# Kernel optimization log

Hardware: AMD Instinct MI355X
Metric: run time of the kernel (lower is better)

## Reference

```python
import jax, jax.numpy as jnp
import numpy as np
import math

# Module hyperparameters (match init_kwargs)
N_LEVELS = 16
LOG2_T = 19
T = 2 ** LOG2_T
BASE = (16, 16)
FINEST = (512, 512)
NUM_HASHGRID = 2
N_POINTS = 1_000_000
PRIME_Y = np.uint32(2654435761)  # standard NGP spatial-hash prime for the 2nd dim


def _resolutions():
    # replicate torch: int(base * b**i) per axis
    b_w = math.exp((math.log(FINEST[0]) - math.log(BASE[0])) / (N_LEVELS - 1))
    b_h = math.exp((math.log(FINEST[1]) - math.log(BASE[1])) / (N_LEVELS - 1))
    res_w = [int(BASE[0] * b_w ** i) for i in range(N_LEVELS)]
    res_h = [int(BASE[1] * b_h ** i) for i in range(N_LEVELS)]
    return jnp.array(np.stack([res_w, res_h], axis=-1), dtype=jnp.int32)  # [L,2]


def setup_inputs() -> dict:
    key = jax.random.key(0)
    k1, k2, k3 = jax.random.split(key, 3)
    x = jax.random.uniform(k1, (N_POINTS, 2), dtype=jnp.float32)
    hash_idxs = jax.random.randint(k2, (N_POINTS, 1), 0, NUM_HASHGRID, dtype=jnp.int32)
    # xavier-normal-like init of the hash tables [G, L, T, F]
    fan_in = N_LEVELS * T * 2
    fan_out = NUM_HASHGRID * T * 2
    std = math.sqrt(2.0 / (fan_in + fan_out))
    features = jax.random.normal(k3, (NUM_HASHGRID, N_LEVELS, T, 2), dtype=jnp.float32) * std
    return {"x": x, "features": features, "hash_idxs": hash_idxs}


def reference(x, features, hash_idxs):
    N = x.shape[0]
    res = _resolutions()                              # [L,2] int32
    scale = (res - 1).astype(jnp.float32)             # [L,2]
    pos = x[:, None, :] * scale[None]                 # [N,L,2]
    i0f = jnp.floor(pos)
    w = pos - i0f                                     # bilinear fractions [N,L,2]
    i0 = i0f.astype(jnp.int32).astype(jnp.uint32)     # [N,L,2]

    # 4 corner offsets: (0,0),(1,0),(0,1),(1,1)
    offs = jnp.array([[0, 0], [1, 0], [0, 1], [1, 1]], dtype=jnp.uint32)  # [4,2]
    corners = i0[:, :, None, :] + offs[None, None]    # [N,L,4,2]
    # NGP spatial hash, modulo table size via mask (T is power of 2)
    h = (corners[..., 0] ^ (corners[..., 1] * PRIME_Y)) & np.uint32(T - 1)  # [N,L,4]
    h = h.astype(jnp.int32)

    g = hash_idxs.reshape(-1)                         # [N] which hash grid
    lidx = jnp.arange(N_LEVELS, dtype=jnp.int32)
    feat = features[g[:, None, None], lidx[None, :, None], h]  # [N,L,4,2]

    wx, wy = w[..., 0], w[..., 1]
    wc = jnp.stack([(1 - wx) * (1 - wy), wx * (1 - wy), (1 - wx) * wy, wx * wy], axis=-1)  # [N,L,4]
    out = jnp.einsum('nlc,nlcf->nlf', wc, feat)       # [N,L,2]
    return out.reshape(N, N_LEVELS * 2)
```

## Files before the change

kernel.cpp:

```cpp
#include <hip/hip_runtime.h>
#include <math.h>

#define NL 16
#define TS (1u << 19)
#define TMASK (TS - 1u)
#define PRIME 2654435761u

#define NBINS 8192
#define BIN_GBIT 12

struct ScalePack { float s[NL]; };

__device__ __forceinline__ unsigned bin_of(float px, float py, int g) {
    int iy = (int)(py * 511.0f); iy = iy < 0 ? 0 : (iy > 511 ? 511 : iy);
    int ix = (int)(px * 511.0f); ix = ix < 0 ? 0 : (ix > 511 ? 511 : ix);
    return ((unsigned)g << BIN_GBIT) | ((unsigned)iy << 3) | ((unsigned)ix >> 6);
}

__global__ __launch_bounds__(256)
void k_zero(unsigned* __restrict__ p, int n) {
    int i = blockIdx.x * blockDim.x + threadIdx.x;
    if (i < n) p[i] = 0u;
}

__global__ __launch_bounds__(256)
void k_hist(const float2* __restrict__ x, const int* __restrict__ hidx,
            unsigned* __restrict__ hist, int N)
{
    int n = blockIdx.x * blockDim.x + threadIdx.x;
    if (n >= N) return;
    float2 p = x[n];
    atomicAdd(&hist[bin_of(p.x, p.y, hidx[n])], 1u);
}

__global__ __launch_bounds__(1024)
void k_scan(const unsigned* __restrict__ hist, unsigned* __restrict__ offs)
{
    __shared__ unsigned partial[1024];
    int t = threadIdx.x;
    unsigned v[8];
    unsigned s = 0;
    #pragma unroll
    for (int i = 0; i < 8; ++i) { v[i] = hist[t * 8 + i]; s += v[i]; }
    partial[t] = s;
    __syncthreads();
    for (int d = 1; d < 1024; d <<= 1) {
        unsigned add = (t >= d) ? partial[t - d] : 0u;
        __syncthreads();
        partial[t] += add;
        __syncthreads();
    }
    unsigned base = (t == 0) ? 0u : partial[t - 1];
    #pragma unroll
    for (int i = 0; i < 8; ++i) { offs[t * 8 + i] = base; base += v[i]; }
}

__global__ __launch_bounds__(256)
void k_scatter(const float2* __restrict__ x, const int* __restrict__ hidx,
               unsigned* __restrict__ offs,
               float2* __restrict__ sxy, unsigned* __restrict__ smeta, int N)
{
    int n = blockIdx.x * blockDim.x + threadIdx.x;
    if (n >= N) return;
    float2 p = x[n];
    int g = hidx[n];
    unsigned b = bin_of(p.x, p.y, g);
    unsigned pos = atomicAdd(&offs[b], 1u);
    sxy[pos] = p;
    smeta[pos] = (unsigned)n | ((unsigned)g << 24);
}

__global__ __launch_bounds__(256)
void hashgrid2d_sorted(const float2* __restrict__ sxy,
                       const unsigned* __restrict__ smeta,
                       const float2* __restrict__ feat,
                       float4* __restrict__ out,
                       ScalePack sp, int N)
{
    int nwg = gridDim.x;
    int orig = blockIdx.x;
    int q = nwg >> 3, r = nwg & 7;
    int xcd = orig & 7, loc = orig >> 3;
    int bid = (xcd < r ? xcd * (q + 1) : r * (q + 1) + (xcd - r) * q) + loc;

    int n = bid * 256 + (int)threadIdx.x;
    if (n >= N) return;

    float2 p = sxy[n];
    unsigned meta = smeta[n];
    int g  = (int)(meta >> 24);
    int no = (int)(meta & 0xFFFFFFu);
    float px = p.x, py = p.y;
    const float2* fb = feat + (size_t)g * ((size_t)NL * TS);

    float of[2 * NL];

    #pragma unroll 4
    for (int l = 0; l < NL; ++l) {
        float s  = sp.s[l];
        float fx = px * s;
        float fy = py * s;
        float fx0 = floorf(fx), fy0 = floorf(fy);
        float wx = fx - fx0, wy = fy - fy0;
        unsigned ix = (unsigned)(int)fx0;
        unsigned iy = (unsigned)(int)fy0;
        unsigned hy0 = iy * PRIME;
        unsigned hy1 = (iy + 1u) * PRIME;

        const float2* tab = fb + (size_t)l * TS;
        float2 c00 = tab[( ix       ^ hy0) & TMASK];
        float2 c10 = tab[((ix + 1u) ^ hy0) & TMASK];
        float2 c01 = tab[( ix       ^ hy1) & TMASK];
        float2 c11 = tab[((ix + 1u) ^ hy1) & TMASK];

        float w00 = (1.f - wx) * (1.f - wy);
        float w10 = wx * (1.f - wy);
        float w01 = (1.f - wx) * wy;
        float w11 = wx * wy;

        of[2 * l]     = w00 * c00.x + w10 * c10.x + w01 * c01.x + w11 * c11.x;
        of[2 * l + 1] = w00 * c00.y + w10 * c10.y + w01 * c01.y + w11 * c11.y;
    }

    float4* op = out + (size_t)no * 8;
    #pragma unroll
    for (int qq = 0; qq < 8; ++qq)
        op[qq] = make_float4(of[4 * qq], of[4 * qq + 1], of[4 * qq + 2], of[4 * qq + 3]);
}

__global__ __launch_bounds__(256)
void hashgrid2d_fwd(const float2* __restrict__ x,
                    const float2* __restrict__ feat,
                    const int* __restrict__ hidx,
                    float4* __restrict__ out,
                    ScalePack sp, int N)
{
    int n = blockIdx.x * blockDim.x + threadIdx.x;
    if (n >= N) return;

    float2 p = x[n];
    float px = p.x, py = p.y;
    int g = hidx[n];
    const float2* fb = feat + (size_t)g * ((size_t)NL * TS);

    float of[2 * NL];

    #pragma unroll 4
    for (int l = 0; l < NL; ++l) {
        float s  = sp.s[l];
        float fx = px * s;
        float fy = py * s;
        float fx0 = floorf(fx), fy0 = floorf(fy);
        float wx = fx - fx0, wy = fy - fy0;
        unsigned ix = (unsigned)(int)fx0;
        unsigned iy = (unsigned)(int)fy0;
        unsigned hy0 = iy * PRIME;
        unsigned hy1 = (iy + 1u) * PRIME;

        const float2* tab = fb + (size_t)l * TS;
        float2 c00 = tab[( ix       ^ hy0) & TMASK];
        float2 c10 = tab[((ix + 1u) ^ hy0) & TMASK];
        float2 c01 = tab[( ix       ^ hy1) & TMASK];
        float2 c11 = tab[((ix + 1u) ^ hy1) & TMASK];

        float w00 = (1.f - wx) * (1.f - wy);
        float w10 = wx * (1.f - wy);
        float w01 = (1.f - wx) * wy;
        float w11 = wx * wy;

        of[2 * l]     = w00 * c00.x + w10 * c10.x + w01 * c01.x + w11 * c11.x;
        of[2 * l + 1] = w00 * c00.y + w10 * c10.y + w01 * c01.y + w11 * c11.y;
    }

    float4* op = out + (size_t)n * 8;
    #pragma unroll
    for (int qq = 0; qq < 8; ++qq)
        op[qq] = make_float4(of[4 * qq], of[4 * qq + 1], of[4 * qq + 2], of[4 * qq + 3]);
}

extern "C" void kernel_launch(void* const* d_in, const int* in_sizes, int n_in,
                              void* d_out, int out_size, void* d_ws, size_t ws_size,
                              hipStream_t stream) {
    const float2* x    = (const float2*)d_in[0];
    const float2* feat = (const float2*)d_in[1];
    const int*    hidx = (const int*)d_in[2];
    int N = in_sizes[0] / 2;

    ScalePack sp;
    double b = exp((log(512.0) - log(16.0)) / 15.0);
    for (int i = 0; i < NL; ++i) {
        int r = (int)(16.0 * pow(b, (double)i));
        sp.s[i] = (float)(r - 1);
    }

    int threads = 256;
    int blocks = (N + threads - 1) / threads;

    size_t histB = (size_t)NBINS * 4;
    size_t offB  = (size_t)NBINS * 4;
    size_t xyB   = (size_t)N * 8;
    size_t metaB = (size_t)N * 4;
    size_t need  = histB + offB + xyB + metaB;

    if (d_ws != nullptr && ws_size >= need) {
        unsigned* hist  = (unsigned*)d_ws;
        unsigned* offs  = hist + NBINS;
        float2*   sxy   = (float2*)((char*)d_ws + histB + offB);
        unsigned* smeta = (unsigned*)((char*)d_ws + histB + offB + xyB);

        hipLaunchKernelGGL(k_zero, dim3((NBINS + 255) / 256), dim3(256), 0, stream,
                           hist, NBINS);
        hipLaunchKernelGGL(k_hist, dim3(blocks), dim3(threads), 0, stream,
                           x, hidx, hist, N);
        hipLaunchKernelGGL(k_scan, dim3(1), dim3(1024), 0, stream, hist, offs);
        hipLaunchKernelGGL(k_scatter, dim3(blocks), dim3(threads), 0, stream,
                           x, hidx, offs, sxy, smeta, N);
        hipLaunchKernelGGL(hashgrid2d_sorted, dim3(blocks), dim3(threads), 0, stream,
                           sxy, smeta, feat, (float4*)d_out, sp, N);
    } else {
        hipLaunchKernelGGL(hashgrid2d_fwd, dim3(blocks), dim3(threads), 0, stream,
                           x, feat, hidx, (float4*)d_out, sp, N);
    }
}
```

Baseline: 353.3 us.

## Fuse sort preprocessing into one cooperative kernel and use nontemporal output stores

The four binning kernels (zero, histogram, scan, scatter) are replaced by one cooperative kernel that uses grid-wide syncs and keeps each thread's two points in registers across phases, so x and hidx are read once and three launches go away. The scan now runs in a single block inside that kernel. A fallback keeps the old multi-kernel path if the cooperative launch is unavailable. Output stores in the sorted gather kernel become nontemporal vector stores to avoid polluting cache with write-only data. Grid syncs add barrier cost, and the single-block scan stalls the rest of the grid.

```diff
diff --git a/kernel.cpp b/kernel.cpp
--- a/kernel.cpp
+++ b/kernel.cpp
@@ -1,5 +1,8 @@
 #include <hip/hip_runtime.h>
+#include <hip/hip_cooperative_groups.h>
 #include <math.h>
+
+namespace cg = cooperative_groups;
 
 #define NL 16
 #define TS (1u << 19)
@@ -9,12 +12,75 @@
 #define NBINS 8192
 #define BIN_GBIT 12
 
+typedef float f4 __attribute__((ext_vector_type(4)));
+
 struct ScalePack { float s[NL]; };
 
 __device__ __forceinline__ unsigned bin_of(float px, float py, int g) {
     int iy = (int)(py * 511.0f); iy = iy < 0 ? 0 : (iy > 511 ? 511 : iy);
     int ix = (int)(px * 511.0f); ix = ix < 0 ? 0 : (ix > 511 ? 511 : ix);
     return ((unsigned)g << BIN_GBIT) | ((unsigned)iy << 3) | ((unsigned)ix >> 6);
+}
+
+__global__ __launch_bounds__(256, 8)
+void k_prep(const float2* __restrict__ x, const int* __restrict__ hidx,
+            unsigned* __restrict__ hist,
+            float2* __restrict__ sxy, unsigned* __restrict__ smeta, int N)
+{
+    cg::grid_group grid = cg::this_grid();
+    int tid = blockIdx.x * 256 + threadIdx.x;
+    int nth = gridDim.x * 256;
+
+    for (int i = tid; i < NBINS; i += nth) hist[i] = 0u;
+    grid.sync();
+
+    float2 p0, p1; int g0 = 0, g1 = 0; unsigned b0 = 0, b1 = 0;
+    int n0 = -1, n1 = -1;
+    int i0 = tid, i1 = tid + nth;
+    if (i0 < N) {
+        p0 = x[i0]; g0 = hidx[i0]; b0 = bin_of(p0.x, p0.y, g0); n0 = i0;
+        atomicAdd(&hist[b0], 1u);
+    }
+    if (i1 < N) {
+        p1 = x[i1]; g1 = hidx[i1]; b1 = bin_of(p1.x, p1.y, g1); n1 = i1;
+        atomicAdd(&hist[b1], 1u);
+    }
+    grid.sync();
+
+    if (blockIdx.x == 0) {
+        __shared__ unsigned part[256];
+        unsigned v[32];
+        unsigned s = 0;
+        #pragma unroll
+        for (int i = 0; i < 32; ++i) { v[i] = hist[threadIdx.x * 32 + i]; s += v[i]; }
+        part[threadIdx.x] = s;
+        __syncthreads();
+        for (int d = 1; d < 256; d <<= 1) {
+            unsigned add = (threadIdx.x >= (unsigned)d) ? part[threadIdx.x - d] : 0u;
+            __syncthreads();
+            part[threadIdx.x] += add;
+            __syncthreads();
+        }
+        unsigned base = threadIdx.x ? part[threadIdx.x - 1] : 0u;
+        #pragma unroll
+        for (int i = 0; i < 32; ++i) {
+            unsigned c = v[i];
+            hist[threadIdx.x * 32 + i] = base;
+            base += c;
+        }
+    }
+    grid.sync();
+
+    if (n0 >= 0) {
+        unsigned pos = atomicAdd(&hist[b0], 1u);
+        sxy[pos] = p0;
+        smeta[pos] = (unsigned)n0 | ((unsigned)g0 << 24);
+    }
+    if (n1 >= 0) {
+        unsigned pos = atomicAdd(&hist[b1], 1u);
+        sxy[pos] = p1;
+        smeta[pos] = (unsigned)n1 | ((unsigned)g1 << 24);
+    }
 }
 
 __global__ __launch_bounds__(256)
@@ -122,10 +188,12 @@
         of[2 * l + 1] = w00 * c00.y + w10 * c10.y + w01 * c01.y + w11 * c11.y;
     }
 
-    float4* op = out + (size_t)no * 8;
+    f4* op = reinterpret_cast<f4*>(out + (size_t)no * 8);
     #pragma unroll
-    for (int qq = 0; qq < 8; ++qq)
-        op[qq] = make_float4(of[4 * qq], of[4 * qq + 1], of[4 * qq + 2], of[4 * qq + 3]);
+    for (int qq = 0; qq < 8; ++qq) {
+        f4 v = { of[4 * qq], of[4 * qq + 1], of[4 * qq + 2], of[4 * qq + 3] };
+        __builtin_nontemporal_store(v, op + qq);
+    }
 }
 
 __global__ __launch_bounds__(256)
@@ -208,13 +276,43 @@
         float2*   sxy   = (float2*)((char*)d_ws + histB + offB);
         unsigned* smeta = (unsigned*)((char*)d_ws + histB + offB + xyB);
 
-        hipLaunchKernelGGL(k_zero, dim3((NBINS + 255) / 256), dim3(256), 0, stream,
-                           hist, NBINS);
-        hipLaunchKernelGGL(k_hist, dim3(blocks), dim3(threads), 0, stream,
-                           x, hidx, hist, N);
-        hipLaunchKernelGGL(k_scan, dim3(1), dim3(1024), 0, stream, hist, offs);
-        hipLaunchKernelGGL(k_scatter, dim3(blocks), dim3(threads), 0, stream,
-                           x, hidx, offs, sxy, smeta, N);
+        static int coopGrid = -2;
+        if (coopGrid == -2) {
+            int nCU = 0, occ = 0;
+            if (hipDeviceGetAttribute(&nCU, hipDeviceAttributeMultiprocessorCount, 0)
+                    == hipSuccess &&
+                hipOccupancyMaxActiveBlocksPerMultiprocessor(
+                    &occ, (const void*)k_prep, 256, 0) == hipSuccess &&
+                nCU > 0 && occ > 0)
+                coopGrid = nCU * occ;
+            else
+                coopGrid = -1;
+        }
+
+        bool coop_ok = false;
+        if (coopGrid > 0) {
+            int grid = coopGrid > 2048 ? 2048 : coopGrid;
+            if ((size_t)grid * 512 >= (size_t)N) {
+                const float2* xa = x; const int* ha = hidx;
+                unsigned* hi = hist; float2* sa = sxy; unsigned* sm = smeta; int Na = N;
+                void* args[] = { &xa, &ha, &hi, &sa, &sm, &Na };
+                if (hipLaunchCooperativeKernel((const void*)k_prep, dim3(grid),
+                                               dim3(256), args, 0, stream)
+                        == hipSuccess)
+                    coop_ok = true;
+            }
+        }
+
+        if (!coop_ok) {
+            hipLaunchKernelGGL(k_zero, dim3((NBINS + 255) / 256), dim3(256), 0, stream,
+                               hist, NBINS);
+            hipLaunchKernelGGL(k_hist, dim3(blocks), dim3(threads), 0, stream,
+                               x, hidx, hist, N);
+            hipLaunchKernelGGL(k_scan, dim3(1), dim3(1024), 0, stream, hist, offs);
+            hipLaunchKernelGGL(k_scatter, dim3(blocks), dim3(threads), 0, stream,
+                               x, hidx, offs, sxy, smeta, N);
+        }
+
         hipLaunchKernelGGL(hashgrid2d_sorted, dim3(blocks), dim3(threads), 0, stream,
                            sxy, smeta, feat, (float4*)d_out, sp, N);
     } else {
```

New measurement: 530.3 us. +50.1%, slower.

## Replace counting sort with fixed-capacity bin slots and overflow region

Applied to the files above, without the earlier changes.

Drops the histogram and scan passes and replaces them with direct placement into fixed-capacity per-bin slots (CAP=192), plus an atomic-indexed overflow area for bins that fill up. The main kernel now launches over all slots, returns early for empty ones, and rereads x by original index instead of keeping a sorted xy copy. Output stores become nontemporal. The aim is to cut kernel launches, one full pass over the input, and scan latency. In exchange it launches many more threads (about 1.57M slots plus N), many of which exit immediately, and the x gathers are less coalesced.

```diff
diff --git a/kernel.cpp b/kernel.cpp
--- a/kernel.cpp
+++ b/kernel.cpp
@@ -8,6 +8,10 @@
 
 #define NBINS 8192
 #define BIN_GBIT 12
+#define CAP 192
+#define SLOTS (NBINS * CAP)
+
+typedef float f4 __attribute__((ext_vector_type(4)));
 
 struct ScalePack { float s[NL]; };
 
@@ -24,58 +28,32 @@
 }
 
 __global__ __launch_bounds__(256)
-void k_hist(const float2* __restrict__ x, const int* __restrict__ hidx,
-            unsigned* __restrict__ hist, int N)
-{
-    int n = blockIdx.x * blockDim.x + threadIdx.x;
-    if (n >= N) return;
-    float2 p = x[n];
-    atomicAdd(&hist[bin_of(p.x, p.y, hidx[n])], 1u);
-}
-
-__global__ __launch_bounds__(1024)
-void k_scan(const unsigned* __restrict__ hist, unsigned* __restrict__ offs)
-{
-    __shared__ unsigned partial[1024];
-    int t = threadIdx.x;
-    unsigned v[8];
-    unsigned s = 0;
-    #pragma unroll
-    for (int i = 0; i < 8; ++i) { v[i] = hist[t * 8 + i]; s += v[i]; }
-    partial[t] = s;
-    __syncthreads();
-    for (int d = 1; d < 1024; d <<= 1) {
-        unsigned add = (t >= d) ? partial[t - d] : 0u;
-        __syncthreads();
-        partial[t] += add;
-        __syncthreads();
-    }
-    unsigned base = (t == 0) ? 0u : partial[t - 1];
-    #pragma unroll
-    for (int i = 0; i < 8; ++i) { offs[t * 8 + i] = base; base += v[i]; }
-}
-
-__global__ __launch_bounds__(256)
-void k_scatter(const float2* __restrict__ x, const int* __restrict__ hidx,
-               unsigned* __restrict__ offs,
-               float2* __restrict__ sxy, unsigned* __restrict__ smeta, int N)
+void k_place(const float2* __restrict__ x, const int* __restrict__ hidx,
+             unsigned* __restrict__ cur, unsigned* __restrict__ smeta, int N)
 {
     int n = blockIdx.x * blockDim.x + threadIdx.x;
     if (n >= N) return;
     float2 p = x[n];
     int g = hidx[n];
     unsigned b = bin_of(p.x, p.y, g);
-    unsigned pos = atomicAdd(&offs[b], 1u);
-    sxy[pos] = p;
-    smeta[pos] = (unsigned)n | ((unsigned)g << 24);
-}
-
-__global__ __launch_bounds__(256)
-void hashgrid2d_sorted(const float2* __restrict__ sxy,
-                       const unsigned* __restrict__ smeta,
-                       const float2* __restrict__ feat,
-                       float4* __restrict__ out,
-                       ScalePack sp, int N)
+    unsigned pos = atomicAdd(&cur[b], 1u);
+    unsigned slot;
+    if (pos < CAP) {
+        slot = b * CAP + pos;
+    } else {
+        unsigned o = atomicAdd(&cur[NBINS], 1u);
+        slot = (unsigned)SLOTS + o;
+    }
+    smeta[slot] = (unsigned)n | ((unsigned)g << 24);
+}
+
+__global__ __launch_bounds__(256)
+void hashgrid2d_slots(const unsigned* __restrict__ smeta,
+                      const unsigned* __restrict__ cnt,
+                      const float2* __restrict__ x,
+                      const float2* __restrict__ feat,
+                      float4* __restrict__ out,
+                      ScalePack sp, int N)
 {
     int nwg = gridDim.x;
     int orig = blockIdx.x;
@@ -83,13 +61,25 @@
     int xcd = orig & 7, loc = orig >> 3;
     int bid = (xcd < r ? xcd * (q + 1) : r * (q + 1) + (xcd - r) * q) + loc;
 
-    int n = bid * 256 + (int)threadIdx.x;
-    if (n >= N) return;
-
-    float2 p = sxy[n];
-    unsigned meta = smeta[n];
+    int idx = bid * 256 + (int)threadIdx.x;
+
+    unsigned meta;
+    if (idx < SLOTS) {
+        unsigned bin  = (unsigned)idx / CAP;
+        unsigned slot = (unsigned)idx - bin * CAP;
+        unsigned c = cnt[bin];
+        if (c > CAP) c = CAP;
+        if (slot >= c) return;
+        meta = smeta[idx];
+    } else {
+        unsigned ov = (unsigned)(idx - SLOTS);
+        if (ov >= cnt[NBINS]) return;
+        meta = smeta[idx];
+    }
+
     int g  = (int)(meta >> 24);
     int no = (int)(meta & 0xFFFFFFu);
+    float2 p = x[no];
     float px = p.x, py = p.y;
     const float2* fb = feat + (size_t)g * ((size_t)NL * TS);
 
@@ -122,10 +112,12 @@
         of[2 * l + 1] = w00 * c00.y + w10 * c10.y + w01 * c01.y + w11 * c11.y;
     }
 
-    float4* op = out + (size_t)no * 8;
+    f4* op = reinterpret_cast<f4*>(out + (size_t)no * 8);
     #pragma unroll
-    for (int qq = 0; qq < 8; ++qq)
-        op[qq] = make_float4(of[4 * qq], of[4 * qq + 1], of[4 * qq + 2], of[4 * qq + 3]);
+    for (int qq = 0; qq < 8; ++qq) {
+        f4 v = { of[4 * qq], of[4 * qq + 1], of[4 * qq + 2], of[4 * qq + 3] };
+        __builtin_nontemporal_store(v, op + qq);
+    }
 }
 
 __global__ __launch_bounds__(256)
@@ -196,27 +188,22 @@
     int threads = 256;
     int blocks = (N + threads - 1) / threads;
 
-    size_t histB = (size_t)NBINS * 4;
-    size_t offB  = (size_t)NBINS * 4;
-    size_t xyB   = (size_t)N * 8;
-    size_t metaB = (size_t)N * 4;
-    size_t need  = histB + offB + xyB + metaB;
-
-    if (d_ws != nullptr && ws_size >= need) {
-        unsigned* hist  = (unsigned*)d_ws;
-        unsigned* offs  = hist + NBINS;
-        float2*   sxy   = (float2*)((char*)d_ws + histB + offB);
-        unsigned* smeta = (unsigned*)((char*)d_ws + histB + offB + xyB);
-
-        hipLaunchKernelGGL(k_zero, dim3((NBINS + 255) / 256), dim3(256), 0, stream,
-                           hist, NBINS);
-        hipLaunchKernelGGL(k_hist, dim3(blocks), dim3(threads), 0, stream,
-                           x, hidx, hist, N);
-        hipLaunchKernelGGL(k_scan, dim3(1), dim3(1024), 0, stream, hist, offs);
-        hipLaunchKernelGGL(k_scatter, dim3(blocks), dim3(threads), 0, stream,
-                           x, hidx, offs, sxy, smeta, N);
-        hipLaunchKernelGGL(hashgrid2d_sorted, dim3(blocks), dim3(threads), 0, stream,
-                           sxy, smeta, feat, (float4*)d_out, sp, N);
+    size_t curB  = 65536;
+    size_t metaB = ((size_t)SLOTS + (size_t)N) * 4;
+    size_t need  = curB + metaB;
+
+    if (d_ws != nullptr && ws_size >= need && N < (1 << 24)) {
+        unsigned* cur   = (unsigned*)d_ws;
+        unsigned* smeta = (unsigned*)((char*)d_ws + curB);
+
+        hipLaunchKernelGGL(k_zero, dim3((NBINS + 1 + 255) / 256), dim3(256), 0, stream,
+                           cur, NBINS + 1);
+        hipLaunchKernelGGL(k_place, dim3(blocks), dim3(threads), 0, stream,
+                           x, hidx, cur, smeta, N);
+        int total = SLOTS + N;
+        int mblocks = (total + threads - 1) / threads;
+        hipLaunchKernelGGL(hashgrid2d_slots, dim3(mblocks), dim3(threads), 0, stream,
+                           smeta, cur, x, feat, (float4*)d_out, sp, N);
     } else {
         hipLaunchKernelGGL(hashgrid2d_fwd, dim3(blocks), dim3(threads), 0, stream,
                            x, feat, hidx, (float4*)d_out, sp, N);
```

Result: slower. 447.7 us (+26.7%).
